# Optimization experiments

Hardware: AMD Instinct MI355X
Metric: run time of the kernel (lower is better)

## Reference

```python
import jax, jax.numpy as jnp
import numpy as np
from functools import partial

EPS = 1e-5

def batchnorm(x, gamma, beta):
    # training-mode BN over (N,H,W) per channel, NCHW layout
    mean = jnp.mean(x, axis=(0, 2, 3), keepdims=True)
    var = jnp.var(x, axis=(0, 2, 3), keepdims=True)
    xn = (x - mean) * jax.lax.rsqrt(var + EPS)
    return xn * gamma[None, :, None, None] + beta[None, :, None, None]

def ternarize(w):
    # TBN-style per-output-filter ternary quantization: {-a,0,+a}
    absw = jnp.abs(w)
    delta = 0.7 * jnp.mean(absw, axis=(1, 2, 3), keepdims=True)
    mask = (absw > delta).astype(w.dtype)
    alpha = jnp.sum(absw * mask, axis=(1, 2, 3), keepdims=True) / (
        jnp.sum(mask, axis=(1, 2, 3), keepdims=True) + 1e-8)
    return jnp.sign(w) * mask * alpha

def conv(x, w, stride, padding):
    return jax.lax.conv_general_dilated(
        x, w, window_strides=(stride, stride),
        padding=[(padding, padding), (padding, padding)],
        dimension_numbers=("NCHW", "OIHW", "NCHW"))


def setup_inputs() -> dict:
    key = jax.random.key(0)
    ks = jax.random.split(key, 8)
    in_planes, planes, stride = 512, 256, 2
    out_planes = planes * 4
    d = dict(
        x=jax.random.normal(ks[0], (64, in_planes, 28, 28), dtype=jnp.float32),
        bn1_g=jnp.ones((in_planes,), jnp.float32),
        bn1_b=jnp.zeros((in_planes,), jnp.float32),
        w1=jax.random.normal(ks[1], (planes, in_planes, 1, 1), jnp.float32) * 0.05,
        bn2_g=jnp.ones((planes,), jnp.float32),
        bn2_b=jnp.zeros((planes,), jnp.float32),
        w2=jax.random.normal(ks[2], (planes, planes, 3, 3), jnp.float32) * 0.05,
        bn3_g=jnp.ones((planes,), jnp.float32),
        bn3_b=jnp.zeros((planes,), jnp.float32),
        w3=jax.random.normal(ks[3], (out_planes, planes, 1, 1), jnp.float32) * 0.05,
        ds_w=jax.random.normal(ks[4], (out_planes, in_planes, 1, 1), jnp.float32) * 0.05,
        ds_bn_g=jnp.ones((out_planes,), jnp.float32),
        ds_bn_b=jnp.zeros((out_planes,), jnp.float32),
    )
    return d


def reference(x, bn1_g, bn1_b, w1, bn2_g, bn2_b, w2, bn3_g, bn3_b, w3,
              ds_w, ds_bn_g, ds_bn_b):
    stride = 2
    identity = x
    # pre-activation chain: BN -> ternary-quantized conv
    h = conv(batchnorm(x, bn1_g, bn1_b), ternarize(w1), 1, 0)          # [N,256,28,28]
    h = conv(batchnorm(h, bn2_g, bn2_b), ternarize(w2), stride, 1)     # [N,256,14,14]
    h = conv(batchnorm(h, bn3_g, bn3_b), ternarize(w3), 1, 0)          # [N,1024,14,14]
    # downsample(identity, x): projected shortcut + residual add
    sc = batchnorm(conv(identity, ds_w, stride, 0), ds_bn_g, ds_bn_b)
    return h + sc
```

## Files before the change

### kernel.cpp

```cpp
#include <hip/hip_runtime.h>
#include <hip/hip_bf16.h>
#include <math.h>

#define EPS 1e-5f

typedef __hip_bfloat16 bf16;
typedef short short8 __attribute__((ext_vector_type(8)));
typedef float float4v __attribute__((ext_vector_type(4)));

__device__ __forceinline__ float toF(float v) { return v; }
__device__ __forceinline__ float toF(bf16 v) { return __bfloat162float(v); }
__device__ __forceinline__ void stF(float* p, float v) { *p = v; }
__device__ __forceinline__ void stF(bf16* p, float v) { *p = __float2bfloat16(v); }
__device__ __forceinline__ short f2bs(float v) {
    bf16 b = __float2bfloat16(v);
    return *reinterpret_cast<short*>(&b);
}
__device__ __forceinline__ float bs2f(short s) {
    unsigned u = ((unsigned)(unsigned short)s) << 16;
    return __uint_as_float(u);
}

__device__ __forceinline__ void gload_lds16(const short* g, short* l) {
    __builtin_amdgcn_global_load_lds(
        (const __attribute__((address_space(1))) unsigned int*)g,
        (__attribute__((address_space(3))) unsigned int*)l, 16, 0, 0);
}

__device__ __forceinline__ float block_reduce_sum(float v) {
    __shared__ float s[256];
    int t = threadIdx.x;
    s[t] = v;
    __syncthreads();
    #pragma unroll
    for (int st = 128; st > 0; st >>= 1) {
        if (t < st) s[t] += s[t + st];
        __syncthreads();
    }
    float r = s[0];
    __syncthreads();
    return r;
}

__global__ void ternarize_kernel(const float* __restrict__ w, short* __restrict__ wt,
                                 float* __restrict__ alpha, int K) {
    int f = blockIdx.x;
    const float* wf = w + (size_t)f * K;
    short* wtf = wt + (size_t)f * K;

    float s = 0.f;
    for (int i = threadIdx.x; i < K; i += blockDim.x) s += fabsf(wf[i]);
    float total = block_reduce_sum(s);
    float delta = 0.7f * total / (float)K;

    float sm = 0.f, cm = 0.f;
    for (int i = threadIdx.x; i < K; i += blockDim.x) {
        float a = fabsf(wf[i]);
        if (a > delta) { sm += a; cm += 1.f; }
    }
    sm = block_reduce_sum(sm);
    cm = block_reduce_sum(cm);
    if (threadIdx.x == 0) alpha[f] = sm / (cm + 1e-8f);

    for (int i = threadIdx.x; i < K; i += blockDim.x) {
        float v = wf[i];
        float a = fabsf(v);
        wtf[i] = (a > delta) ? ((v > 0.f) ? (short)0x3F80 : (short)0xBF80) : (short)0;
    }
}

__global__ void foldbias_kernel(const short* __restrict__ wt, const float* __restrict__ scale,
                                const float* __restrict__ shift, short* __restrict__ wf,
                                float* __restrict__ bias, int K) {
    int f = blockIdx.x;
    float s = 0.f;
    for (int k = threadIdx.x; k < K; k += blockDim.x) {
        float tv = bs2f(wt[(size_t)f * K + k]);
        wf[(size_t)f * K + k] = f2bs(tv * scale[k]);
        s += tv * shift[k];
    }
    s = block_reduce_sum(s);
    if (threadIdx.x == 0) bias[f] = s;
}

__global__ void f2bf_kernel(const float* __restrict__ in, short* __restrict__ out, int n) {
    int i = blockIdx.x * blockDim.x + threadIdx.x;
    if (i < n) out[i] = f2bs(in[i]);
}

template <typename T, int VEC>
__global__ __launch_bounds__(256) void bn_sum_kernel(
    const T* __restrict__ src, float* __restrict__ sum, float* __restrict__ sq,
    int C, int spatial, int N, int splits) {
    int c = blockIdx.x;
    int vpc = spatial / VEC;
    int total = N * vpc;
    float s = 0.f, s2 = 0.f;
    for (int v = blockIdx.y * 256 + threadIdx.x; v < total; v += splits * 256) {
        int n = v / vpc;
        int i = v - n * vpc;
        const T* p = src + ((size_t)n * C + c) * spatial + i * VEC;
        float vals[VEC];
        if (sizeof(T) == 4) {
            float4 q = *(const float4*)p;
            vals[0] = q.x; vals[1] = q.y; vals[2] = q.z; vals[3] = q.w;
        } else {
            short tmp[VEC];
            if (VEC == 8) *(int4*)tmp = *(const int4*)p;
            else          *(int2*)tmp = *(const int2*)p;
            #pragma unroll
            for (int k = 0; k < VEC; k++) vals[k] = bs2f(tmp[k]);
        }
        #pragma unroll
        for (int k = 0; k < VEC; k++) { s += vals[k]; s2 += vals[k] * vals[k]; }
    }
    s = block_reduce_sum(s);
    s2 = block_reduce_sum(s2);
    if (threadIdx.x == 0) {
        atomicAdd(&sum[c], s);
        atomicAdd(&sq[c], s2);
    }
}

__global__ void bn_finalize_kernel(const float* __restrict__ sum, const float* __restrict__ sq,
                                   const float* __restrict__ g, const float* __restrict__ b,
                                   float* __restrict__ scale, float* __restrict__ shift,
                                   int C, float cnt) {
    int c = blockIdx.x * blockDim.x + threadIdx.x;
    if (c >= C) return;
    float mean = sum[c] / cnt;
    float var = fmaxf(sq[c] / cnt - mean * mean, 0.f);
    float r = rsqrtf(var + EPS);
    float sc = g[c] * r;
    scale[c] = sc;
    shift[c] = b[c] - mean * sc;
}

__global__ __launch_bounds__(256) void stats_transpose_kernel(
    const float* __restrict__ in, short* __restrict__ Bt,
    float* __restrict__ sum, float* __restrict__ sq, int C, int SP) {
    __shared__ short tile[64][66];
    __shared__ float rs[4][64], rq[4][64];
    int n = blockIdx.z;
    int ci0 = blockIdx.y * 64;
    int p0 = blockIdx.x * 64;
    int t = threadIdx.x;
    int tx = t & 63;
    int ty4 = t >> 6;

    {
        int p4 = t & 15;
        int cib = t >> 4;
        int p = p0 + p4 * 4;
        bool pok = (p + 3) < SP;
        #pragma unroll
        for (int it = 0; it < 4; it++) {
            int ci = cib + it * 16;
            float4 q;
            if (pok) q = *(const float4*)(in + ((size_t)n * C + ci0 + ci) * SP + p);
            else     q = make_float4(0.f, 0.f, 0.f, 0.f);
            tile[p4 * 4 + 0][ci] = f2bs(q.x);
            tile[p4 * 4 + 1][ci] = f2bs(q.y);
            tile[p4 * 4 + 2][ci] = f2bs(q.z);
            tile[p4 * 4 + 3][ci] = f2bs(q.w);
        }
    }
    __syncthreads();

    {
        int seg = t & 7;
        #pragma unroll
        for (int it = 0; it < 2; it++) {
            int pl = (t >> 3) + it * 32;
            int pw = p0 + pl;
            if (pw < SP) {
                short v[8];
                #pragma unroll
                for (int u = 0; u < 8; u++) v[u] = tile[pl][seg * 8 + u];
                *(int4*)(Bt + ((size_t)n * SP + pw) * C + ci0 + seg * 8) = *(int4*)v;
            }
        }
    }

    float s = 0.f, s2 = 0.f;
    #pragma unroll
    for (int r = 0; r < 16; r++) {
        int pl = ty4 + r * 4;
        int pw = p0 + pl;
        if (pw < SP) {
            float v = bs2f(tile[pl][tx]);
            s += v; s2 += v * v;
        }
    }
    rs[ty4][tx] = s; rq[ty4][tx] = s2;
    __syncthreads();
    if (ty4 == 0) {
        float ts = rs[0][tx] + rs[1][tx] + rs[2][tx] + rs[3][tx];
        float tq = rq[0][tx] + rq[1][tx] + rq[2][tx] + rq[3][tx];
        atomicAdd(&sum[ci0 + tx], ts);
        atomicAdd(&sq[ci0 + tx], tq);
    }
}

__global__ __launch_bounds__(256) void affine_transpose_bf16_kernel(
    const bf16* __restrict__ in, const float* __restrict__ scale,
    const float* __restrict__ shift, short* __restrict__ Bt,
    int C, int SP) {
    __shared__ short tile[64][66];
    int n = blockIdx.z;
    int ci0 = blockIdx.y * 64;
    int p0 = blockIdx.x * 64;
    int t = threadIdx.x;

    {
        int p4 = t & 15;
        int cib = t >> 4;
        int p = p0 + p4 * 4;
        bool pok = (p + 3) < SP;
        #pragma unroll
        for (int it = 0; it < 4; it++) {
            int ci = cib + it * 16;
            short v[4] = {0, 0, 0, 0};
            if (pok) *(int2*)v = *(const int2*)(in + ((size_t)n * C + ci0 + ci) * SP + p);
            float sc = scale[ci0 + ci], sh = shift[ci0 + ci];
            #pragma unroll
            for (int j = 0; j < 4; j++)
                tile[p4 * 4 + j][ci] = f2bs(bs2f(v[j]) * sc + sh);
        }
    }
    __syncthreads();

    {
        int seg = t & 7;
        #pragma unroll
        for (int it = 0; it < 2; it++) {
            int pl = (t >> 3) + it * 32;
            int pw = p0 + pl;
            if (pw < SP) {
                short v[8];
                #pragma unroll
                for (int u = 0; u < 8; u++) v[u] = tile[pl][seg * 8 + u];
                *(int4*)(Bt + ((size_t)n * SP + pw) * C + ci0 + seg * 8) = *(int4*)v;
            }
        }
    }
}

__global__ __launch_bounds__(256) void im2col_tiled_kernel(
    const bf16* __restrict__ h1, const float* __restrict__ scale,
    const float* __restrict__ shift, short* __restrict__ B2t) {
    __shared__ short tile[16][784];
    int cb = blockIdx.x;
    int n  = blockIdx.y;
    int ci0 = cb * 16;
    int t = threadIdx.x;

    for (int v = t; v < 16 * 98; v += 256) {
        int ci = v / 98;
        int i8 = (v - ci * 98) * 8;
        short tmp[8];
        *(int4*)tmp = *(const int4*)(h1 + ((size_t)n * 256 + ci0 + ci) * 784 + i8);
        float sc = scale[ci0 + ci], sh = shift[ci0 + ci];
        short ov[8];
        #pragma unroll
        for (int k = 0; k < 8; k++) ov[k] = f2bs(bs2f(tmp[k]) * sc + sh);
        *(int4*)&tile[ci][i8] = *(int4*)ov;
    }
    __syncthreads();

    for (int w = t; w < 196 * 18; w += 256) {
        int p = w / 18, seg = w - p * 18;
        int oh = p / 14, ow = p - oh * 14;
        int kbase = seg * 8;
        short vals[8];
        #pragma unroll
        for (int u = 0; u < 8; u++) {
            int kk = kbase + u;
            int ci_l = kk / 9;
            int rr = kk - ci_l * 9;
            int kh = rr / 3, kw = rr - kh * 3;
            int ih = 2 * oh - 1 + kh;
            int iw = 2 * ow - 1 + kw;
            vals[u] = ((unsigned)ih < 28u && (unsigned)iw < 28u)
                          ? tile[ci_l][ih * 28 + iw] : (short)0;
        }
        *(int4*)(B2t + ((size_t)(n * 196 + p)) * 2304 + ci0 * 9 + kbase) = *(int4*)vals;
    }
}

template <int SP, typename TOut, bool HAS_ALPHA, bool FUSE, bool HAS_BIAS, bool BREMAP>
__global__ __launch_bounds__(256) void gemm_kernel(
    const short* __restrict__ A, const short* __restrict__ Bt,
    const float* __restrict__ alpha, TOut* __restrict__ out,
    int M, int K,
    const bf16* __restrict__ scv, const float* __restrict__ fscale,
    const float* __restrict__ fshift, const float* __restrict__ bias) {
    __shared__ short As[128 * 32];
    __shared__ short Bs[128 * 32];
    int t = threadIdx.x;
    int c0 = blockIdx.x * 128;
    int m0 = blockIdx.y * 128;
    int w = t >> 6, l = t & 63;
    int wm = (w >> 1) * 64, wn = (w & 1) * 64;

    int r0 = t >> 2;
    int kg = (t & 3) * 8;
    int wbase = w * 512;

    size_t rowB0, rowB1;
    if (BREMAP) {
        int c = c0 + r0;
        int nn = c / 196, pp = c - nn * 196;
        int oh = pp / 14, ow = pp - oh * 14;
        rowB0 = (size_t)nn * 784 + oh * 56 + ow * 2;
        c += 64;
        nn = c / 196; pp = c - nn * 196;
        oh = pp / 14; ow = pp - oh * 14;
        rowB1 = (size_t)nn * 784 + oh * 56 + ow * 2;
    } else {
        rowB0 = c0 + r0;
        rowB1 = c0 + r0 + 64;
    }

    float4v acc[4][4];
    #pragma unroll
    for (int i = 0; i < 4; i++)
        #pragma unroll
        for (int j = 0; j < 4; j++) acc[i][j] = (float4v)0.f;

    int lm = (l >> 4);
    int lc = l & 15;

    for (int k0 = 0; k0 < K; k0 += 32) {
        gload_lds16(A + (size_t)(m0 + r0) * K + k0 + kg,      &As[wbase]);
        gload_lds16(A + (size_t)(m0 + r0 + 64) * K + k0 + kg, &As[2048 + wbase]);
        gload_lds16(Bt + rowB0 * K + k0 + kg,                 &Bs[wbase]);
        gload_lds16(Bt + rowB1 * K + k0 + kg,                 &Bs[2048 + wbase]);
        __syncthreads();

        short8 af[4], bfr[4];
        #pragma unroll
        for (int i = 0; i < 4; i++)
            af[i] = *(const short8*)&As[(wm + i * 16 + lc) * 32 + lm * 8];
        #pragma unroll
        for (int j = 0; j < 4; j++)
            bfr[j] = *(const short8*)&Bs[(wn + j * 16 + lc) * 32 + lm * 8];
        #pragma unroll
        for (int i = 0; i < 4; i++)
            #pragma unroll
            for (int j = 0; j < 4; j++)
                acc[i][j] = __builtin_amdgcn_mfma_f32_16x16x32_bf16(af[i], bfr[j], acc[i][j], 0, 0, 0);
        __syncthreads();
    }

    #pragma unroll
    for (int i = 0; i < 4; i++) {
        #pragma unroll
        for (int r = 0; r < 4; r++) {
            int m = m0 + wm + i * 16 + lm * 4 + r;
            float a = HAS_ALPHA ? alpha[m] : 1.f;
            float bia = HAS_BIAS ? bias[m] : 0.f;
            float fsc = FUSE ? fscale[m] : 0.f;
            float fsh = FUSE ? fshift[m] : 0.f;
            #pragma unroll
            for (int j = 0; j < 4; j++) {
                int c = c0 + wn + j * 16 + lc;
                int n = c / SP;
                int p = c - n * SP;
                size_t idx = ((size_t)n * M + m) * SP + p;
                float v = acc[i][j][r];
                if (HAS_BIAS) v += bia;
                if (HAS_ALPHA) v *= a;
                if (FUSE) v += toF(scv[idx]) * fsc + fsh;
                stF(&out[idx], v);
            }
        }
    }
}

__global__ __launch_bounds__(256) void gemm2_kernel(
    const short* __restrict__ A, const short* __restrict__ Bt,
    const float* __restrict__ alpha, bf16* __restrict__ out,
    int M, int K) {
    constexpr int SP = 196;
    __shared__ short As[64 * 32];
    __shared__ short Bs[64 * 32];
    int t = threadIdx.x;
    int c0 = blockIdx.x * 64;
    int m0 = blockIdx.y * 64;
    int w = t >> 6, l = t & 63;
    int wm = (w >> 1) * 32, wn = (w & 1) * 32;

    int r0 = t >> 2;
    int kg = (t & 3) * 8;
    int wbase = w * 512;

    float4v acc[2][2];
    #pragma unroll
    for (int i = 0; i < 2; i++)
        #pragma unroll
        for (int j = 0; j < 2; j++) acc[i][j] = (float4v)0.f;

    int lm = (l >> 4);
    int lc = l & 15;

    for (int k0 = 0; k0 < K; k0 += 32) {
        gload_lds16(A + (size_t)(m0 + r0) * K + k0 + kg,  &As[wbase]);
        gload_lds16(Bt + (size_t)(c0 + r0) * K + k0 + kg, &Bs[wbase]);
        __syncthreads();

        short8 af[2], bfr[2];
        #pragma unroll
        for (int i = 0; i < 2; i++)
            af[i] = *(const short8*)&As[(wm + i * 16 + lc) * 32 + lm * 8];
        #pragma unroll
        for (int j = 0; j < 2; j++)
            bfr[j] = *(const short8*)&Bs[(wn + j * 16 + lc) * 32 + lm * 8];
        #pragma unroll
        for (int i = 0; i < 2; i++)
            #pragma unroll
            for (int j = 0; j < 2; j++)
                acc[i][j] = __builtin_amdgcn_mfma_f32_16x16x32_bf16(af[i], bfr[j], acc[i][j], 0, 0, 0);
        __syncthreads();
    }

    #pragma unroll
    for (int i = 0; i < 2; i++) {
        #pragma unroll
        for (int r = 0; r < 4; r++) {
            int m = m0 + wm + i * 16 + lm * 4 + r;
            float a = alpha[m];
            #pragma unroll
            for (int j = 0; j < 2; j++) {
                int c = c0 + wn + j * 16 + lc;
                int n = c / SP;
                int p = c - n * SP;
                out[((size_t)n * M + m) * SP + p] = __float2bfloat16(acc[i][j][r] * a);
            }
        }
    }
}

extern "C" void kernel_launch(void* const* d_in, const int* in_sizes, int n_in,
                              void* d_out, int out_size, void* d_ws, size_t ws_size,
                              hipStream_t stream) {
    const float* x      = (const float*)d_in[0];
    const float* bn1_g  = (const float*)d_in[1];
    const float* bn1_b  = (const float*)d_in[2];
    const float* w1     = (const float*)d_in[3];
    const float* bn2_g  = (const float*)d_in[4];
    const float* bn2_b  = (const float*)d_in[5];
    const float* w2     = (const float*)d_in[6];
    const float* bn3_g  = (const float*)d_in[7];
    const float* bn3_b  = (const float*)d_in[8];
    const float* w3     = (const float*)d_in[9];
    const float* ds_w   = (const float*)d_in[10];
    const float* dbn_g  = (const float*)d_in[11];
    const float* dbn_b  = (const float*)d_in[12];
    float* out = (float*)d_out;

    const int N = 64, C1 = 512, C2 = 256, C3 = 1024;
    const int SP1 = 784, SP2 = 196;
    const int NT1 = N * SP1;
    const int NT2 = N * SP2;

    char* wsb = (char*)d_ws;
    size_t off = 0;
    auto alloc = [&](size_t bytes) { char* p = wsb + off; off += (bytes + 255) & ~(size_t)255; return p; };

    char* pool = alloc((size_t)NT2 * 2304 * 2);
    short* B1t = (short*)pool;
    short* B2t = (short*)pool;
    short* B3t = (short*)pool;
    bf16*  sc  = (bf16*)alloc((size_t)N * C3 * SP2 * 2);

    bf16* h1 = (bf16*)alloc((size_t)N * C2 * SP1 * 2);
    bf16* h2 = (bf16*)alloc((size_t)N * C2 * SP2 * 2);
    short* w1t  = (short*)alloc((size_t)C2 * C1 * 2);
    short* w1f  = (short*)alloc((size_t)C2 * C1 * 2);
    short* w2t  = (short*)alloc((size_t)C2 * C2 * 9 * 2);
    short* w3t  = (short*)alloc((size_t)C3 * C2 * 2);
    short* dswb = (short*)alloc((size_t)C3 * C1 * 2);
    float* alpha1 = (float*)alloc(C2 * 4);
    float* alpha2 = (float*)alloc(C2 * 4);
    float* alpha3 = (float*)alloc(C3 * 4);
    float* bias1  = (float*)alloc(C2 * 4);
    float* scale1 = (float*)alloc(C1 * 4);
    float* shift1 = (float*)alloc(C1 * 4);
    float* scale2 = (float*)alloc(C2 * 4);
    float* shift2 = (float*)alloc(C2 * 4);
    float* scale3 = (float*)alloc(C2 * 4);
    float* shift3 = (float*)alloc(C2 * 4);
    float* scaled = (float*)alloc(C3 * 4);
    float* shiftd = (float*)alloc(C3 * 4);
    float* acc_base = (float*)alloc((size_t)(C1 + C2 + C2 + C3) * 2 * 4);
    float* sum1 = acc_base;            float* sq1 = sum1 + C1;
    float* sum2 = sq1 + C1;            float* sq2 = sum2 + C2;
    float* sum3 = sq2 + C2;            float* sq3 = sum3 + C2;
    float* sumd = sq3 + C2;            float* sqd = sumd + C3;
    (void)ws_size; (void)in_sizes; (void)n_in; (void)out_size;

    hipMemsetAsync(acc_base, 0, (size_t)(C1 + C2 + C2 + C3) * 2 * 4, stream);

    ternarize_kernel<<<C2, 256, 0, stream>>>(w1, w1t, alpha1, C1);
    ternarize_kernel<<<C2, 256, 0, stream>>>(w2, w2t, alpha2, C2 * 9);
    ternarize_kernel<<<C3, 256, 0, stream>>>(w3, w3t, alpha3, C2);
    f2bf_kernel<<<(C3 * C1 + 255) / 256, 256, 0, stream>>>(ds_w, dswb, C3 * C1);

    {
        dim3 grid((SP1 + 63) / 64, C1 / 64, N);
        stats_transpose_kernel<<<grid, 256, 0, stream>>>(x, B1t, sum1, sq1, C1, SP1);
    }
    bn_finalize_kernel<<<(C1 + 255) / 256, 256, 0, stream>>>(sum1, sq1, bn1_g, bn1_b,
                                                             scale1, shift1, C1, (float)(N * SP1));
    foldbias_kernel<<<C2, 256, 0, stream>>>(w1t, scale1, shift1, w1f, bias1, C1);

    gemm_kernel<784, bf16, true, false, true, false><<<dim3(NT1 / 128, C2 / 128), 256, 0, stream>>>(
        w1f, B1t, alpha1, h1, C2, C1, nullptr, nullptr, nullptr, bias1);

    gemm_kernel<196, bf16, false, false, false, true><<<dim3(NT2 / 128, C3 / 128), 256, 0, stream>>>(
        dswb, B1t, nullptr, sc, C3, C1, nullptr, nullptr, nullptr, nullptr);

    bn_sum_kernel<bf16, 4><<<dim3(C3, 4), 256, 0, stream>>>(sc, sumd, sqd, C3, SP2, N, 4);
    bn_finalize_kernel<<<(C3 + 255) / 256, 256, 0, stream>>>(sumd, sqd, dbn_g, dbn_b,
                                                             scaled, shiftd, C3, (float)(N * SP2));

    bn_sum_kernel<bf16, 8><<<dim3(C2, 8), 256, 0, stream>>>(h1, sum2, sq2, C2, SP1, N, 8);
    bn_finalize_kernel<<<(C2 + 255) / 256, 256, 0, stream>>>(sum2, sq2, bn2_g, bn2_b,
                                                             scale2, shift2, C2, (float)(N * SP1));
    im2col_tiled_kernel<<<dim3(16, 64), 256, 0, stream>>>(h1, scale2, shift2, B2t);

    gemm2_kernel<<<dim3(NT2 / 64, C2 / 64), 256, 0, stream>>>(
        w2t, B2t, alpha2, h2, C2, C2 * 9);

    bn_sum_kernel<bf16, 4><<<dim3(C2, 4), 256, 0, stream>>>(h2, sum3, sq3, C2, SP2, N, 4);
    bn_finalize_kernel<<<(C2 + 255) / 256, 256, 0, stream>>>(sum3, sq3, bn3_g, bn3_b,
                                                             scale3, shift3, C2, (float)(N * SP2));
    {
        dim3 grid((SP2 + 63) / 64, C2 / 64, N);
        affine_transpose_bf16_kernel<<<grid, 256, 0, stream>>>(
            h2, scale3, shift3, B3t, C2, SP2);
    }

    gemm_kernel<196, float, true, true, false, false><<<dim3(NT2 / 128, C3 / 128), 256, 0, stream>>>(
        w3t, B3t, alpha3, out, C3, C2, sc, scaled, shiftd, nullptr);
}
```

Measured before the change: 428.5 us.

## Fuse BatchNorm sum and sum-of-squares statistics into GEMM epilogues

Removes the three standalone bn_sum passes over h1, sc and h2. The GEMM epilogues now accumulate per-channel sum and sum-of-squares of the bf16-rounded outputs. Partial sums are reduced with wave shuffles and LDS atomics, then added to global with one atomic per channel per block. This avoids re-reading the intermediates from memory, at the cost of extra epilogue work, LDS usage and global atomic contention across many blocks.

```diff
diff --git a/kernel.cpp b/kernel.cpp
--- a/kernel.cpp
+++ b/kernel.cpp
@@ -86,40 +86,6 @@
 __global__ void f2bf_kernel(const float* __restrict__ in, short* __restrict__ out, int n) {
     int i = blockIdx.x * blockDim.x + threadIdx.x;
     if (i < n) out[i] = f2bs(in[i]);
-}
-
-template <typename T, int VEC>
-__global__ __launch_bounds__(256) void bn_sum_kernel(
-    const T* __restrict__ src, float* __restrict__ sum, float* __restrict__ sq,
-    int C, int spatial, int N, int splits) {
-    int c = blockIdx.x;
-    int vpc = spatial / VEC;
-    int total = N * vpc;
-    float s = 0.f, s2 = 0.f;
-    for (int v = blockIdx.y * 256 + threadIdx.x; v < total; v += splits * 256) {
-        int n = v / vpc;
-        int i = v - n * vpc;
-        const T* p = src + ((size_t)n * C + c) * spatial + i * VEC;
-        float vals[VEC];
-        if (sizeof(T) == 4) {
-            float4 q = *(const float4*)p;
-            vals[0] = q.x; vals[1] = q.y; vals[2] = q.z; vals[3] = q.w;
-        } else {
-            short tmp[VEC];
-            if (VEC == 8) *(int4*)tmp = *(const int4*)p;
-            else          *(int2*)tmp = *(const int2*)p;
-            #pragma unroll
-            for (int k = 0; k < VEC; k++) vals[k] = bs2f(tmp[k]);
-        }
-        #pragma unroll
-        for (int k = 0; k < VEC; k++) { s += vals[k]; s2 += vals[k] * vals[k]; }
-    }
-    s = block_reduce_sum(s);
-    s2 = block_reduce_sum(s2);
-    if (threadIdx.x == 0) {
-        atomicAdd(&sum[c], s);
-        atomicAdd(&sq[c], s2);
-    }
 }
 
 __global__ void bn_finalize_kernel(const float* __restrict__ sum, const float* __restrict__ sq,
@@ -288,15 +254,17 @@
     }
 }
 
-template <int SP, typename TOut, bool HAS_ALPHA, bool FUSE, bool HAS_BIAS, bool BREMAP>
+template <int SP, typename TOut, bool HAS_ALPHA, bool FUSE, bool HAS_BIAS, bool BREMAP, bool STATS>
 __global__ __launch_bounds__(256) void gemm_kernel(
     const short* __restrict__ A, const short* __restrict__ Bt,
     const float* __restrict__ alpha, TOut* __restrict__ out,
     int M, int K,
     const bf16* __restrict__ scv, const float* __restrict__ fscale,
-    const float* __restrict__ fshift, const float* __restrict__ bias) {
+    const float* __restrict__ fshift, const float* __restrict__ bias,
+    float* __restrict__ statSum, float* __restrict__ statSq) {
     __shared__ short As[128 * 32];
     __shared__ short Bs[128 * 32];
+    __shared__ float sSum[128], sSq[128];
     int t = threadIdx.x;
     int c0 = blockIdx.x * 128;
     int m0 = blockIdx.y * 128;
@@ -353,6 +321,11 @@
         __syncthreads();
     }
 
+    if (STATS) {
+        if (t < 128) { sSum[t] = 0.f; sSq[t] = 0.f; }
+        __syncthreads();
+    }
+
     #pragma unroll
     for (int i = 0; i < 4; i++) {
         #pragma unroll
@@ -362,6 +335,7 @@
             float bia = HAS_BIAS ? bias[m] : 0.f;
             float fsc = FUSE ? fscale[m] : 0.f;
             float fsh = FUSE ? fshift[m] : 0.f;
+            float ps = 0.f, pq = 0.f;
             #pragma unroll
             for (int j = 0; j < 4; j++) {
                 int c = c0 + wn + j * 16 + lc;
@@ -373,7 +347,31 @@
                 if (HAS_ALPHA) v *= a;
                 if (FUSE) v += toF(scv[idx]) * fsc + fsh;
                 stF(&out[idx], v);
-            }
+                if (STATS) {
+                    float rv = bs2f(f2bs(v));
+                    ps += rv; pq += rv * rv;
+                }
+            }
+            if (STATS) {
+                #pragma unroll
+                for (int msk = 1; msk < 16; msk <<= 1) {
+                    ps += __shfl_xor(ps, msk);
+                    pq += __shfl_xor(pq, msk);
+                }
+                if (lc == 0) {
+                    int ml = wm + i * 16 + lm * 4 + r;
+                    atomicAdd(&sSum[ml], ps);
+                    atomicAdd(&sSq[ml], pq);
+                }
+            }
+        }
+    }
+
+    if (STATS) {
+        __syncthreads();
+        if (t < 128) {
+            atomicAdd(&statSum[m0 + t], sSum[t]);
+            atomicAdd(&statSq[m0 + t], sSq[t]);
         }
     }
 }
@@ -381,10 +379,11 @@
 __global__ __launch_bounds__(256) void gemm2_kernel(
     const short* __restrict__ A, const short* __restrict__ Bt,
     const float* __restrict__ alpha, bf16* __restrict__ out,
-    int M, int K) {
+    int M, int K, float* __restrict__ statSum, float* __restrict__ statSq) {
     constexpr int SP = 196;
     __shared__ short As[64 * 32];
     __shared__ short Bs[64 * 32];
+    __shared__ float sSum[64], sSq[64];
     int t = threadIdx.x;
     int c0 = blockIdx.x * 64;
     int m0 = blockIdx.y * 64;
@@ -424,20 +423,43 @@
         __syncthreads();
     }
 
+    if (t < 64) { sSum[t] = 0.f; sSq[t] = 0.f; }
+    __syncthreads();
+
     #pragma unroll
     for (int i = 0; i < 2; i++) {
         #pragma unroll
         for (int r = 0; r < 4; r++) {
             int m = m0 + wm + i * 16 + lm * 4 + r;
             float a = alpha[m];
+            float ps = 0.f, pq = 0.f;
             #pragma unroll
             for (int j = 0; j < 2; j++) {
                 int c = c0 + wn + j * 16 + lc;
                 int n = c / SP;
                 int p = c - n * SP;
-                out[((size_t)n * M + m) * SP + p] = __float2bfloat16(acc[i][j][r] * a);
-            }
-        }
+                float v = acc[i][j][r] * a;
+                out[((size_t)n * M + m) * SP + p] = __float2bfloat16(v);
+                float rv = bs2f(f2bs(v));
+                ps += rv; pq += rv * rv;
+            }
+            #pragma unroll
+            for (int msk = 1; msk < 16; msk <<= 1) {
+                ps += __shfl_xor(ps, msk);
+                pq += __shfl_xor(pq, msk);
+            }
+            if (lc == 0) {
+                int ml = wm + i * 16 + lm * 4 + r;
+                atomicAdd(&sSum[ml], ps);
+                atomicAdd(&sSq[ml], pq);
+            }
+        }
+    }
+
+    __syncthreads();
+    if (t < 64) {
+        atomicAdd(&statSum[m0 + t], sSum[t]);
+        atomicAdd(&statSq[m0 + t], sSq[t]);
     }
 }
 
@@ -515,25 +537,24 @@
                                                              scale1, shift1, C1, (float)(N * SP1));
     foldbias_kernel<<<C2, 256, 0, stream>>>(w1t, scale1, shift1, w1f, bias1, C1);
 
-    gemm_kernel<784, bf16, true, false, true, false><<<dim3(NT1 / 128, C2 / 128), 256, 0, stream>>>(
-        w1f, B1t, alpha1, h1, C2, C1, nullptr, nullptr, nullptr, bias1);
-
-    gemm_kernel<196, bf16, false, false, false, true><<<dim3(NT2 / 128, C3 / 128), 256, 0, stream>>>(
-        dswb, B1t, nullptr, sc, C3, C1, nullptr, nullptr, nullptr, nullptr);
-
-    bn_sum_kernel<bf16, 4><<<dim3(C3, 4), 256, 0, stream>>>(sc, sumd, sqd, C3, SP2, N, 4);
+    gemm_kernel<784, bf16, true, false, true, false, true>
+        <<<dim3(NT1 / 128, C2 / 128), 256, 0, stream>>>(
+        w1f, B1t, alpha1, h1, C2, C1, nullptr, nullptr, nullptr, bias1, sum2, sq2);
+
+    gemm_kernel<196, bf16, false, false, false, true, true>
+        <<<dim3(NT2 / 128, C3 / 128), 256, 0, stream>>>(
+        dswb, B1t, nullptr, sc, C3, C1, nullptr, nullptr, nullptr, nullptr, sumd, sqd);
+
     bn_finalize_kernel<<<(C3 + 255) / 256, 256, 0, stream>>>(sumd, sqd, dbn_g, dbn_b,
                                                              scaled, shiftd, C3, (float)(N * SP2));
 
-    bn_sum_kernel<bf16, 8><<<dim3(C2, 8), 256, 0, stream>>>(h1, sum2, sq2, C2, SP1, N, 8);
     bn_finalize_kernel<<<(C2 + 255) / 256, 256, 0, stream>>>(sum2, sq2, bn2_g, bn2_b,
                                                              scale2, shift2, C2, (float)(N * SP1));
     im2col_tiled_kernel<<<dim3(16, 64), 256, 0, stream>>>(h1, scale2, shift2, B2t);
 
     gemm2_kernel<<<dim3(NT2 / 64, C2 / 64), 256, 0, stream>>>(
-        w2t, B2t, alpha2, h2, C2, C2 * 9);
-
-    bn_sum_kernel<bf16, 4><<<dim3(C2, 4), 256, 0, stream>>>(h2, sum3, sq3, C2, SP2, N, 4);
+        w2t, B2t, alpha2, h2, C2, C2 * 9, sum3, sq3);
+
     bn_finalize_kernel<<<(C2 + 255) / 256, 256, 0, stream>>>(sum3, sq3, bn3_g, bn3_b,
                                                              scale3, shift3, C2, (float)(N * SP2));
     {
@@ -542,6 +563,7 @@
             h2, scale3, shift3, B3t, C2, SP2);
     }
 
-    gemm_kernel<196, float, true, true, false, false><<<dim3(NT2 / 128, C3 / 128), 256, 0, stream>>>(
-        w3t, B3t, alpha3, out, C3, C2, sc, scaled, shiftd, nullptr);
-}
+    gemm_kernel<196, float, true, true, false, false, false>
+        <<<dim3(NT2 / 128, C3 / 128), 256, 0, stream>>>(
+        w3t, B3t, alpha3, out, C3, C2, sc, scaled, shiftd, nullptr, nullptr, nullptr);
+}
```

Measured after the change: 437.6 us. 2.1% more time.
